# Optimization experiments

Measured on AMD Instinct MI355X. Metric: run time of the kernel, lower is better.

## Reference

```python
import jax, jax.numpy as jnp
import numpy as np

KAPPA = 5  # kNN neighbors per node (module hardcodes kappas = [5]*B, topk of KAPPA+2)


def build_graph(inputs):
    """Vectorized equivalent of get_graph(): returns flat (src, dst, edge_weight)
    over the B*S node space. Filtered kNN edges (dst < 2) are masked via weight 0,
    which is mathematically identical to removing them (gcn_norm uses edge weights)."""
    B, S, _ = inputs.shape
    diff = inputs[:, :, None, :] - inputs[:, None, :, :]            # [B,S,S,2]
    deltas = jnp.sqrt(jnp.sum(diff * diff, axis=-1))                # torch.cdist
    eye = jnp.eye(S, dtype=bool)
    d = jnp.where(eye[None], jnp.inf, deltas)                       # fill_diagonal_(inf)
    nodes = jnp.arange(2, S, dtype=jnp.int32)                       # non-depot nodes
    # depot edges: 0 -> i  and  i -> 1  for i in [2, S)
    src_dep = jnp.concatenate([jnp.zeros(S - 2, jnp.int32), nodes])
    dst_dep = jnp.concatenate([nodes, jnp.ones(S - 2, jnp.int32)])
    # kNN edges: 7 nearest per non-depot node (diag=inf so i never selected)
    _, idx = jax.lax.top_k(-d[:, 2:, :], KAPPA + 2)                 # [B, S-2, 7]
    src_knn = jnp.broadcast_to(nodes[:, None], (S - 2, KAPPA + 2)).reshape(-1)
    dst_knn = idx.reshape(B, -1).astype(jnp.int32)                  # [B, 7*(S-2)]
    mask_knn = (dst_knn >= 2).astype(jnp.float32)                   # drop depot dsts
    src = jnp.concatenate([jnp.broadcast_to(src_dep[None], (B, src_dep.shape[0])), jnp.broadcast_to(src_knn[None], (B, src_knn.shape[0]))], axis=1)
    dst = jnp.concatenate([jnp.broadcast_to(dst_dep[None], (B, dst_dep.shape[0])), dst_knn], axis=1)
    ew = jnp.concatenate([jnp.ones((B, dst_dep.shape[0]), jnp.float32), mask_knn], axis=1)
    offs = (jnp.arange(B, dtype=jnp.int32) * S)[:, None]            # batch node offset
    return (src + offs).reshape(-1), (dst + offs).reshape(-1), ew.reshape(-1)


def gcn_conv(x, src, dst, norm, self_norm, W, b, N):
    h = x @ W                                                       # GCNConv linear
    agg = jax.ops.segment_sum(h[src] * norm[:, None], dst, num_segments=N)
    agg = agg + h * self_norm[:, None]                              # self-loop term
    return agg + b


def gnn_forward(x, src, dst, ew, W0, b0, W1, b1, W2, b2):
    N = x.shape[0]
    deg = jax.ops.segment_sum(ew, dst, num_segments=N) + 1.0        # +1 self-loop
    dinv = 1.0 / jnp.sqrt(deg)
    norm = dinv[src] * dinv[dst] * ew                               # sym gcn_norm
    self_norm = dinv * dinv
    h = jax.nn.relu(gcn_conv(x, src, dst, norm, self_norm, W0, b0, N))
    h = jax.nn.relu(gcn_conv(h, src, dst, norm, self_norm, W1, b1, N))
    return gcn_conv(h, src, dst, norm, self_norm, W2, b2, N)


def setup_inputs() -> dict:
    B, S, D, H = 64, 1000, 128, 512
    key = jax.random.key(0)
    ks = jax.random.split(key, 12)
    sc = lambda fan_in: 1.0 / np.sqrt(fan_in)
    return {
        "inputs": jax.random.uniform(ks[0], (B, S, 2), jnp.float32),
        "scor": jax.random.uniform(ks[1], (B, S, 1), jnp.float32),
        "Wc": jax.random.normal(ks[2], (2, D), jnp.float32) * sc(2),
        "bc": jax.random.normal(ks[3], (D,), jnp.float32) * 0.01,
        "Ws": jax.random.normal(ks[4], (1, D), jnp.float32) * sc(1),
        "bs": jax.random.normal(ks[5], (D,), jnp.float32) * 0.01,
        "W0": jax.random.normal(ks[6], (D, H), jnp.float32) * sc(D),
        "b0": jnp.zeros((H,), jnp.float32),
        "W1": jax.random.normal(ks[8], (H, H), jnp.float32) * sc(H),
        "b1": jnp.zeros((H,), jnp.float32),
        "W2": jax.random.normal(ks[10], (H, D), jnp.float32) * sc(H),
        "b2": jnp.zeros((D,), jnp.float32),
    }


def reference(inputs, scor, Wc, bc, Ws, bs, W0, b0, W1, b1, W2, b2):
    B, S, _ = inputs.shape
    src, dst, ew = build_graph(inputs)
    x = (inputs @ Wc + bc) + (scor @ Ws + bs)                       # embedded_data
    x = x.reshape(B * S, -1)
    out = gnn_forward(x, src, dst, ew, W0, b0, W1, b1, W2, b2)
    return out.reshape(B, S, -1)
```

## Files before the change

### kernel.cpp

```cpp
#include <hip/hip_runtime.h>

typedef unsigned short u16;
typedef unsigned int u32;
typedef unsigned long long u64;
using short8 = __attribute__((ext_vector_type(8))) short;
using f32x4  = __attribute__((ext_vector_type(4))) float;

constexpr int Bb = 64, Ss = 1000, Dd = 128, Hh = 512;
constexpr int NN = Bb * Ss;
constexpr int NSRC = Ss - 2;

__device__ __forceinline__ float bf2f(u16 h) {
    u32 u = ((u32)h) << 16;
    return __builtin_bit_cast(float, u);
}
__device__ __forceinline__ u16 f2bf(float v) {
    u32 u = __builtin_bit_cast(u32, v);
    u32 r = (u + 0x7FFFu + ((u >> 16) & 1u)) >> 16;
    return (u16)r;
}
__device__ __forceinline__ float4 bf4(ushort4 v) {
    float4 r;
    r.x = bf2f(v.x); r.y = bf2f(v.y); r.z = bf2f(v.z); r.w = bf2f(v.w);
    return r;
}
__device__ __forceinline__ void gl_lds16(const void* g, void* l) {
    __builtin_amdgcn_global_load_lds(
        (const __attribute__((address_space(1))) void*)g,
        (__attribute__((address_space(3))) void*)l, 16, 0, 0);
}
__device__ __forceinline__ void acc8(float (&a)[8], uint4 v, float w) {
    u32 c[4] = {v.x, v.y, v.z, v.w};
#pragma unroll
    for (int k = 0; k < 4; ++k) {
        float lo = __builtin_bit_cast(float, c[k] << 16);
        float hi = __builtin_bit_cast(float, c[k] & 0xFFFF0000u);
        a[2 * k]     += lo * w;
        a[2 * k + 1] += hi * w;
    }
}
__device__ __forceinline__ void unp8(float (&a)[8], uint4 v) {
    u32 c[4] = {v.x, v.y, v.z, v.w};
#pragma unroll
    for (int k = 0; k < 4; ++k) {
        a[2 * k]     = __builtin_bit_cast(float, c[k] << 16);
        a[2 * k + 1] = __builtin_bit_cast(float, c[k] & 0xFFFF0000u);
    }
}

__device__ __forceinline__ u64 umin64(u64 a, u64 b) { return a < b ? a : b; }
__device__ __forceinline__ u64 umax64(u64 a, u64 b) { return a < b ? b : a; }

__device__ __forceinline__ void ins8u(u64 (&bd)[8], u64 v) {
#pragma unroll
    for (int k = 7; k >= 1; --k)
        bd[k] = umin64(umax64(v, bd[k - 1]), bd[k]);
    bd[0] = umin64(v, bd[0]);
}

__device__ __forceinline__ void merge8(u64 (&a)[8], int mask) {
    u64 b[8];
#pragma unroll
    for (int k = 0; k < 8; ++k)
        b[k] = __shfl_xor((unsigned long long)a[k], mask);
    u64 m[8];
#pragma unroll
    for (int k = 0; k < 8; ++k) m[k] = umin64(a[k], b[7 - k]);
#pragma unroll
    for (int k = 0; k < 4; ++k) {
        u64 lo = umin64(m[k], m[k + 4]), hi = umax64(m[k], m[k + 4]);
        m[k] = lo; m[k + 4] = hi;
    }
#pragma unroll
    for (int base = 0; base < 8; base += 4)
#pragma unroll
        for (int k = 0; k < 2; ++k) {
            u64 lo = umin64(m[base + k], m[base + k + 2]);
            u64 hi = umax64(m[base + k], m[base + k + 2]);
            m[base + k] = lo; m[base + k + 2] = hi;
        }
#pragma unroll
    for (int base = 0; base < 8; base += 2) {
        u64 lo = umin64(m[base], m[base + 1]), hi = umax64(m[base], m[base + 1]);
        m[base] = lo; m[base + 1] = hi;
    }
#pragma unroll
    for (int k = 0; k < 8; ++k) a[k] = m[k];
}

__global__ __launch_bounds__(256) void knn_bin_kernel(const float* __restrict__ inputs,
                                                      float2* __restrict__ gsxy,
                                                      u16* __restrict__ gsid,
                                                      int* __restrict__ gcst) {
    __shared__ float px[Ss], py[Ss];
    __shared__ int hist[256];
    __shared__ int cur[256];
    int b = blockIdx.x;
    int tid = threadIdx.x;
    const float* base = inputs + (size_t)b * Ss * 2;
    for (int t = tid; t < Ss; t += 256) { px[t] = base[2 * t]; py[t] = base[2 * t + 1]; }
    hist[tid] = 0;
    __syncthreads();
    for (int t = tid; t < Ss; t += 256) {
        int cx = min(15, (int)(px[t] * 16.0f));
        int cy = min(15, (int)(py[t] * 16.0f));
        atomicAdd(&hist[cy * 16 + cx], 1);
    }
    __syncthreads();
    int cnt = hist[tid];
    for (int s = 1; s < 256; s <<= 1) {
        int u = (tid >= s) ? hist[tid - s] : 0;
        __syncthreads();
        hist[tid] += u;
        __syncthreads();
    }
    int st = hist[tid] - cnt;
    cur[tid] = st;
    gcst[b * 260 + tid] = st;
    if (tid == 0) gcst[b * 260 + 256] = Ss;
    __syncthreads();
    for (int t = tid; t < Ss; t += 256) {
        float x = px[t], y = py[t];
        int cx = min(15, (int)(x * 16.0f));
        int cy = min(15, (int)(y * 16.0f));
        int p = atomicAdd(&cur[cy * 16 + cx], 1);
        gsxy[b * 1000 + p] = make_float2(x, y);
        gsid[b * 1000 + p] = (u16)t;
    }
}

__global__ __launch_bounds__(256) void knn_query_kernel(const float* __restrict__ inputs,
                                                        const float2* __restrict__ gsxy,
                                                        const u16* __restrict__ gsid,
                                                        const int* __restrict__ gcst,
                                                        u16* __restrict__ knn,
                                                        int* __restrict__ indeg) {
    __shared__ float2 sxy[Ss];
    __shared__ u16 sid[Ss];
    __shared__ int cst[257];
    int b = blockIdx.x;
    int tid = threadIdx.x;
    for (int t = tid; t < Ss; t += 256) { sxy[t] = gsxy[b * 1000 + t]; sid[t] = gsid[b * 1000 + t]; }
    for (int t = tid; t < 257; t += 256) cst[t] = gcst[b * 260 + t];
    __syncthreads();

    int sub = tid & 7;
    int g = tid >> 3;
    int i = 2 + blockIdx.y * 32 + g;
    if (i >= Ss) return;

    float x = inputs[(size_t)b * 2000 + 2 * i];
    float y = inputs[(size_t)b * 2000 + 2 * i + 1];
    int cx = min(15, (int)(x * 16.0f));
    int cy = min(15, (int)(y * 16.0f));
    const float INF = __builtin_inff();
    constexpr float h = 0.0625f;

    u64 bd[8];
    int w = 1;
    for (;;) {
#pragma unroll
        for (int k = 0; k < 8; ++k) bd[k] = ~0ULL;
        int x0 = max(0, cx - w), x1 = min(15, cx + w);
        int y0 = max(0, cy - w), y1 = min(15, cy + w);
        for (int cyy = y0; cyy <= y1; ++cyy) {
            int p0 = cst[cyy * 16 + x0];
            int p1 = cst[cyy * 16 + x1 + 1];
            for (int p = p0 + sub; p < p1; p += 8) {
                float2 q = sxy[p];
                int j = sid[p];
                float dx = __fsub_rn(x, q.x);
                float dy = __fsub_rn(y, q.y);
                float d2 = __fadd_rn(__fmul_rn(dx, dx), __fmul_rn(dy, dy));
                float d = __fsqrt_rn(d2);
                u64 key = (((u64)__builtin_bit_cast(u32, d)) << 32) | (u32)j;
                key = (j == i) ? ~0ULL : key;
                ins8u(bd, key);
            }
        }
        merge8(bd, 1); merge8(bd, 2); merge8(bd, 4);
        float d7 = __builtin_bit_cast(float, (u32)(bd[6] >> 32));
        float bL = (x0 > 0)  ? (x - (float)x0 * h) : INF;
        float bR = (x1 < 15) ? ((float)(x1 + 1) * h - x) : INF;
        float bB = (y0 > 0)  ? (y - (float)y0 * h) : INF;
        float bT = (y1 < 15) ? ((float)(y1 + 1) * h - y) : INF;
        float bound = fminf(fminf(bL, bR), fminf(bB, bT));
        if (d7 <= bound - 2e-6f || w >= 16) break;
        ++w;
    }

    if (sub == 0) {
        u16* kp = knn + ((size_t)b * NSRC + (i - 2)) * 7;
#pragma unroll
        for (int k = 0; k < 7; ++k) {
            int j = (int)(u32)bd[k];
            kp[k] = (u16)j;
            if (j >= 2) atomicAdd(&indeg[b * Ss + j], 1);
        }
    }
}

__global__ void deg_dinv_kernel(const int* __restrict__ indeg, float* __restrict__ dinv) {
    int n = blockIdx.x * 256 + threadIdx.x;
    if (n >= NN) return;
    int i = n % Ss;
    float deg = (i == 0) ? 1.0f : (i == 1) ? (float)(Ss - 1) : (float)(indeg[n] + 2);
    dinv[n] = 1.0f / __fsqrt_rn(deg);
}

__global__ __launch_bounds__(1024) void scan1_kernel(const int* __restrict__ indeg,
                                                     int* __restrict__ offs,
                                                     int* __restrict__ bsum) {
    __shared__ int sh[1024];
    int t = threadIdx.x;
    int idx = blockIdx.x * 1024 + t;
    int v = (idx < NN) ? indeg[idx] : 0;
    sh[t] = v;
    __syncthreads();
    for (int off = 1; off < 1024; off <<= 1) {
        int u = (t >= off) ? sh[t - off] : 0;
        __syncthreads();
        sh[t] += u;
        __syncthreads();
    }
    if (idx < NN) offs[idx] = sh[t] - v;
    if (t == 1023) bsum[blockIdx.x] = sh[1023];
}

__global__ void scan2_kernel(int* __restrict__ bsum) {
    if (threadIdx.x == 0) {
        int run = 0;
        for (int k = 0; k < 63; ++k) { int v = bsum[k]; bsum[k] = run; run += v; }
        bsum[63] = run;
    }
}

__global__ __launch_bounds__(1024) void scan3_kernel(int* __restrict__ offs,
                                                     const int* __restrict__ bsum) {
    int idx = blockIdx.x * 1024 + threadIdx.x;
    if (idx < NN) offs[idx] += bsum[blockIdx.x];
    if (idx == 0) offs[NN] = bsum[63];
}

__global__ __launch_bounds__(256) void fill_rev_kernel(const u16* __restrict__ knn,
                                                       const int* __restrict__ offs,
                                                       int* __restrict__ cursor,
                                                       u16* __restrict__ rev) {
    if (threadIdx.x >= 250) return;
    int b = blockIdx.x;
    int i = 2 + blockIdx.y * 250 + threadIdx.x;
    if (i >= Ss) return;
    const u16* kp = knn + ((size_t)b * NSRC + (i - 2)) * 7;
#pragma unroll
    for (int k = 0; k < 7; ++k) {
        int d = kp[k];
        if (d >= 2) {
            int n = b * Ss + d;
            int p = atomicAdd(&cursor[n], 1);
            rev[offs[n] + p] = (u16)i;
        }
    }
}

__global__ __launch_bounds__(512) void fuse0_kernel(const float* __restrict__ Wc,
                                                    const float* __restrict__ bc,
                                                    const float* __restrict__ Ws,
                                                    const float* __restrict__ bs,
                                                    const float* __restrict__ W0,
                                                    float* __restrict__ A) {
    int h = threadIdx.x;
    float a0 = 0.f, a1 = 0.f, a2 = 0.f, a3 = 0.f;
    for (int c = 0; c < Dd; ++c) {
        float w = W0[c * Hh + h];
        a0 += Wc[c] * w;
        a1 += Wc[Dd + c] * w;
        a2 += Ws[c] * w;
        a3 += (bc[c] + bs[c]) * w;
    }
    A[h] = a0; A[Hh + h] = a1; A[2 * Hh + h] = a2; A[3 * Hh + h] = a3;
}

__global__ __launch_bounds__(256) void gemm0f_kernel(const float* __restrict__ inputs,
                                                     const float* __restrict__ scor,
                                                     const float* __restrict__ A,
                                                     u16* __restrict__ Y) {
    int gid = blockIdx.x * 256 + threadIdx.x;
    if (gid >= NN * 128) return;
    int n = gid >> 7, t = gid & 127;
    int h = t * 4;
    float i0 = inputs[2 * n], i1 = inputs[2 * n + 1], sc = scor[n];
    float4 a0 = *(const float4*)(A + h);
    float4 a1 = *(const float4*)(A + Hh + h);
    float4 a2 = *(const float4*)(A + 2 * Hh + h);
    float4 a3 = *(const float4*)(A + 3 * Hh + h);
    ushort4 o;
    o.x = f2bf(i0 * a0.x + i1 * a1.x + sc * a2.x + a3.x);
    o.y = f2bf(i0 * a0.y + i1 * a1.y + sc * a2.y + a3.y);
    o.z = f2bf(i0 * a0.z + i1 * a1.z + sc * a2.z + a3.z);
    o.w = f2bf(i0 * a0.w + i1 * a1.w + sc * a2.w + a3.w);
    *(ushort4*)(Y + (size_t)n * Hh + h) = o;
}

__global__ void transp_kernel(const float* __restrict__ src,
                              u16* __restrict__ dst, int R, int C) {
    int gid = blockIdx.x * 256 + threadIdx.x;
    if (gid >= R * C) return;
    int r = gid / C, c = gid - r * C;
    dst[c * R + r] = f2bf(src[gid]);
}

__global__ __launch_bounds__(256) void gemm_kernel(const u16* __restrict__ A,
                                                   const u16* __restrict__ W,
                                                   u16* __restrict__ Y,
                                                   int K, int Ncols,
                                                   int nyb, int nxb) {
    __shared__ __align__(16) u16 lA[128][64];
    __shared__ __align__(16) u16 lW[128][64];

    int grp = blockIdx.x / (8 * nxb);
    int rem = blockIdx.x - grp * (8 * nxb);
    int xcd = rem & 7;
    int xb  = rem >> 3;
    int yb  = grp * 8 + xcd;
    if (yb >= nyb) return;

    int row0 = yb * 128;
    int col0 = xb * 128;
    int tid = threadIdx.x;
    int lane = tid & 63, wid = tid >> 6;
    int wm = (wid >> 1) * 64, wn = (wid & 1) * 64;
    int lanelo = lane & 15, quad = lane >> 4;

    int lrow = lane >> 3;
    int lslot = lane & 7;

    f32x4 acc[4][4] = {};

    for (int k0 = 0; k0 < K; k0 += 64) {
#pragma unroll
        for (int t = 0; t < 4; ++t) {
            int chunk = t * 4 + wid;
            int row = chunk * 8 + lrow;
            int sc = lslot ^ (row & 7);
            gl_lds16(A + (size_t)(row0 + row) * K + k0 + sc * 8, &lA[chunk * 8][0]);
        }
#pragma unroll
        for (int t = 0; t < 4; ++t) {
            int chunk = t * 4 + wid;
            int row = chunk * 8 + lrow;
            int sc = lslot ^ (row & 7);
            gl_lds16(W + (size_t)(col0 + row) * K + k0 + sc * 8, &lW[chunk * 8][0]);
        }
        __syncthreads();

#pragma unroll
        for (int kk = 0; kk < 64; kk += 32) {
            short8 af[4], bw[4];
            int cbb = (kk >> 3) + quad;
#pragma unroll
            for (int mt = 0; mt < 4; ++mt) {
                int r = wm + mt * 16 + lanelo;
                af[mt] = *(const short8*)&lA[r][((cbb ^ (r & 7))) * 8];
            }
#pragma unroll
            for (int nt = 0; nt < 4; ++nt) {
                int r = wn + nt * 16 + lanelo;
                bw[nt] = *(const short8*)&lW[r][((cbb ^ (r & 7))) * 8];
            }
#pragma unroll
            for (int mt = 0; mt < 4; ++mt)
#pragma unroll
                for (int nt = 0; nt < 4; ++nt)
                    acc[mt][nt] = __builtin_amdgcn_mfma_f32_16x16x32_bf16(
                        af[mt], bw[nt], acc[mt][nt], 0, 0, 0);
        }
        __syncthreads();
    }

#pragma unroll
    for (int mt = 0; mt < 4; ++mt)
#pragma unroll
        for (int nt = 0; nt < 4; ++nt)
#pragma unroll
            for (int r = 0; r < 4; ++r) {
                int row = row0 + wm + mt * 16 + quad * 4 + r;
                int col = col0 + wn + nt * 16 + lanelo;
                Y[(size_t)row * Ncols + col] = f2bf(acc[mt][nt][r]);
            }
}

__global__ __launch_bounds__(1024) void dep1_kernel(const u16* __restrict__ y,
                                                    const float* __restrict__ dinv,
                                                    float* __restrict__ dq,
                                                    int M) {
    int b = blockIdx.x;
    int qq = blockIdx.y;
    int co = blockIdx.z * 128;
    int tid = threadIdx.x;
    int c4 = tid & 31;
    int es = tid >> 5;
    int j0 = 2 + qq * 250;
    int j1 = j0 + 250; if (j1 > Ss) j1 = Ss;
    const u16* yb = y + (size_t)b * Ss * M + co + c4 * 4;
    const float* dv = dinv + b * Ss;
    float a0 = 0.f, a1 = 0.f, a2 = 0.f, a3 = 0.f;
    for (int j = j0 + es; j < j1; j += 32) {
        float w = dv[j];
        float4 u = bf4(*(const ushort4*)(yb + (size_t)j * M));
        a0 += u.x * w; a1 += u.y * w; a2 += u.z * w; a3 += u.w * w;
    }
    __shared__ float4 red[1024];
    float4 mv; mv.x = a0; mv.y = a1; mv.z = a2; mv.w = a3;
    red[tid] = mv;
    __syncthreads();
#pragma unroll
    for (int s = 16; s > 0; s >>= 1) {
        if (es < s) {
            float4 o = red[tid + (s << 5)];
            float4 m = red[tid];
            m.x += o.x; m.y += o.y; m.z += o.z; m.w += o.w;
            red[tid] = m;
        }
        __syncthreads();
    }
    if (es == 0)
        *(float4*)(dq + ((size_t)qq * Bb + b) * M + co + c4 * 4) = red[c4];
}

__global__ __launch_bounds__(256) void aggw512_kernel(const u16* __restrict__ y,
                                                      const float* __restrict__ dinv,
                                                      const int* __restrict__ offs,
                                                      const int* __restrict__ indeg,
                                                      const u16* __restrict__ rev,
                                                      const float* __restrict__ bias,
                                                      const float* __restrict__ dep1,
                                                      u16* __restrict__ oX) {
    int tid = threadIdx.x;
    int wv = tid >> 6, lane = tid & 63;
    int bx = blockIdx.x;
    int b = (bx & 7) + 8 * (bx / 2000);
    int i = ((bx >> 3) % 250) * 4 + wv;
    int nb = b * Ss;
    int n = nb + i;
    const u16* yB = y + (size_t)nb * 512 + lane * 8;

    float acc[8] = {};
    if (i >= 2) {
        int cnt = indeg[n], o = offs[n];
        int rv = 0; float rw = 0.f;
        if (lane < 16 && lane < cnt) { rv = rev[o + lane]; rw = dinv[nb + rv]; }
        float w0 = dinv[nb];
        uint4 v0 = *(const uint4*)yB;
        acc8(acc, v0, w0);
        int cl = cnt < 16 ? cnt : 16;
        int e = 0;
        for (; e + 4 <= cl; e += 4) {
            int   s0 = __shfl(rv, e),     s1 = __shfl(rv, e + 1);
            int   s2 = __shfl(rv, e + 2), s3 = __shfl(rv, e + 3);
            float w_0 = __shfl(rw, e),     w_1 = __shfl(rw, e + 1);
            float w_2 = __shfl(rw, e + 2), w_3 = __shfl(rw, e + 3);
            uint4 u0 = *(const uint4*)(yB + (size_t)s0 * 512);
            uint4 u1 = *(const uint4*)(yB + (size_t)s1 * 512);
            uint4 u2 = *(const uint4*)(yB + (size_t)s2 * 512);
            uint4 u3 = *(const uint4*)(yB + (size_t)s3 * 512);
            acc8(acc, u0, w_0); acc8(acc, u1, w_1);
            acc8(acc, u2, w_2); acc8(acc, u3, w_3);
        }
        for (; e < cl; ++e) {
            int s = __shfl(rv, e); float ww = __shfl(rw, e);
            uint4 u = *(const uint4*)(yB + (size_t)s * 512);
            acc8(acc, u, ww);
        }
        for (; e < cnt; ++e) {
            int s = rev[o + e]; float ww = dinv[nb + s];
            uint4 u = *(const uint4*)(yB + (size_t)s * 512);
            acc8(acc, u, ww);
        }
    } else if (i == 1) {
        const float* dp = dep1 + (size_t)b * 512 + lane * 8;
#pragma unroll
        for (int qq = 0; qq < 4; ++qq) {
            float4 v0 = *(const float4*)(dp + (size_t)qq * Bb * 512);
            float4 v1 = *(const float4*)(dp + (size_t)qq * Bb * 512 + 4);
            acc[0] += v0.x; acc[1] += v0.y; acc[2] += v0.z; acc[3] += v0.w;
            acc[4] += v1.x; acc[5] += v1.y; acc[6] += v1.z; acc[7] += v1.w;
        }
    }
    float dn = dinv[n], sn = dn * dn;
    float s8[8];
    unp8(s8, *(const uint4*)(yB + (size_t)i * 512));
    float4 bl = *(const float4*)(bias + lane * 8);
    float4 bh = *(const float4*)(bias + lane * 8 + 4);
    float bz[8] = {bl.x, bl.y, bl.z, bl.w, bh.x, bh.y, bh.z, bh.w};
    u32 ow[4];
#pragma unroll
    for (int k = 0; k < 4; ++k) {
        float z0 = acc[2 * k]     * dn + s8[2 * k]     * sn + bz[2 * k];
        float z1 = acc[2 * k + 1] * dn + s8[2 * k + 1] * sn + bz[2 * k + 1];
        ow[k] = (u32)f2bf(fmaxf(z0, 0.f)) | ((u32)f2bf(fmaxf(z1, 0.f)) << 16);
    }
    uint4 ov = {ow[0], ow[1], ow[2], ow[3]};
    *(uint4*)(oX + (size_t)n * 512 + lane * 8) = ov;
}

__global__ __launch_bounds__(128) void agg128f_kernel(const u16* __restrict__ y,
                                                      const float* __restrict__ dinv,
                                                      const int* __restrict__ offs,
                                                      const int* __restrict__ indeg,
                                                      const u16* __restrict__ rev,
                                                      const float* __restrict__ bias,
                                                      const float* __restrict__ dep1,
                                                      float* __restrict__ out) {
    int bx = blockIdx.x;
    int x = bx & 7, q = bx >> 3;
    int bb = q / 1000;
    int i = q - bb * 1000;
    int b = x + (bb << 3);
    int n = b * Ss + i;
    int nb = n - i;
    int tid = threadIdx.x, c = tid;

    __shared__ int   sidx[128];
    __shared__ float sw[128];
    int cnt = 0, o = 0;
    if (i >= 2) { cnt = indeg[n]; o = offs[n]; }
    int cl = cnt < 128 ? cnt : 128;
    if (tid < cl) {
        int s = rev[o + tid];
        sidx[tid] = s;
        sw[tid] = dinv[nb + s];
    }
    __syncthreads();

    float a = 0.f;
    if (i >= 2) {
        a = bf2f(y[(size_t)nb * 128 + c]) * dinv[nb];
        int e = 0;
        for (; e + 4 <= cl; e += 4) {
            int s0 = sidx[e], s1 = sidx[e + 1], s2 = sidx[e + 2], s3 = sidx[e + 3];
            float w0 = sw[e], w1 = sw[e + 1], w2 = sw[e + 2], w3 = sw[e + 3];
            float u0 = bf2f(y[(size_t)(nb + s0) * 128 + c]);
            float u1 = bf2f(y[(size_t)(nb + s1) * 128 + c]);
            float u2 = bf2f(y[(size_t)(nb + s2) * 128 + c]);
            float u3 = bf2f(y[(size_t)(nb + s3) * 128 + c]);
            a += u0 * w0 + u1 * w1 + u2 * w2 + u3 * w3;
        }
        for (; e < cl; ++e) a += bf2f(y[(size_t)(nb + sidx[e]) * 128 + c]) * sw[e];
        for (int e2 = 128; e2 < cnt; ++e2) {
            int s = rev[o + e2];
            a += bf2f(y[(size_t)(nb + s) * 128 + c]) * dinv[nb + s];
        }
    } else if (i == 1) {
#pragma unroll
        for (int qq = 0; qq < 4; ++qq)
            a += dep1[((size_t)qq * Bb + b) * 128 + c];
    }
    float dn = dinv[n];
    out[(size_t)n * 128 + c] = a * dn + bf2f(y[(size_t)n * 128 + c]) * (dn * dn) + bias[c];
}

constexpr size_t O_INDEG  = 0;
constexpr size_t O_CURSOR = 256000;
constexpr size_t O_OFFS   = 512000;
constexpr size_t O_DINV   = 768256;
constexpr size_t O_KNN    = 1024256;
constexpr size_t O_REV    = 1918080;
constexpr size_t O_AMAT   = 2811904;
constexpr size_t O_WT1    = 2942976;
constexpr size_t O_WT2    = 3467264;
constexpr size_t O_X      = 3598336;
constexpr size_t O_Y      = 69134336;
constexpr size_t O_DEP1A  = 134670336;
constexpr size_t O_DEP1B  = 135194624;
constexpr size_t O_BSUM   = 135325696;
constexpr size_t O_GSXY   = O_X;
constexpr size_t O_GSID   = O_X + 512000;
constexpr size_t O_GCST   = O_X + 640000;

extern "C" void kernel_launch(void* const* d_in, const int* in_sizes, int n_in,
                              void* d_out, int out_size, void* d_ws, size_t ws_size,
                              hipStream_t stream) {
    const float* inputs = (const float*)d_in[0];
    const float* scor   = (const float*)d_in[1];
    const float* Wc     = (const float*)d_in[2];
    const float* bc     = (const float*)d_in[3];
    const float* Ws     = (const float*)d_in[4];
    const float* bs     = (const float*)d_in[5];
    const float* W0     = (const float*)d_in[6];
    const float* b0     = (const float*)d_in[7];
    const float* W1     = (const float*)d_in[8];
    const float* b1     = (const float*)d_in[9];
    const float* W2     = (const float*)d_in[10];
    const float* b2     = (const float*)d_in[11];

    char* w = (char*)d_ws;
    int*    indeg  = (int*)(w + O_INDEG);
    int*    cursor = (int*)(w + O_CURSOR);
    int*    offs   = (int*)(w + O_OFFS);
    float*  dinv   = (float*)(w + O_DINV);
    u16*    knn    = (u16*)(w + O_KNN);
    u16*    rev    = (u16*)(w + O_REV);
    float*  amat   = (float*)(w + O_AMAT);
    u16*    wt1    = (u16*)(w + O_WT1);
    u16*    wt2    = (u16*)(w + O_WT2);
    u16*    xbf    = (u16*)(w + O_X);
    u16*    ybf    = (u16*)(w + O_Y);
    float*  dep1a  = (float*)(w + O_DEP1A);
    float*  dep1b  = (float*)(w + O_DEP1B);
    int*    bsum   = (int*)(w + O_BSUM);
    float2* gsxy   = (float2*)(w + O_GSXY);
    u16*    gsid   = (u16*)(w + O_GSID);
    int*    gcst   = (int*)(w + O_GCST);

    hipMemsetAsync(w + O_INDEG, 0, 512000, stream);

    knn_bin_kernel<<<Bb, 256, 0, stream>>>(inputs, gsxy, gsid, gcst);
    knn_query_kernel<<<dim3(Bb, 32), 256, 0, stream>>>(inputs, gsxy, gsid, gcst, knn, indeg);
    deg_dinv_kernel<<<250, 256, 0, stream>>>(indeg, dinv);
    scan1_kernel<<<63, 1024, 0, stream>>>(indeg, offs, bsum);
    scan2_kernel<<<1, 64, 0, stream>>>(bsum);
    scan3_kernel<<<63, 1024, 0, stream>>>(offs, bsum);
    fill_rev_kernel<<<dim3(Bb, 4), 256, 0, stream>>>(knn, offs, cursor, rev);

    fuse0_kernel<<<1, 512, 0, stream>>>(Wc, bc, Ws, bs, W0, amat);
    transp_kernel<<<(Hh * Hh + 255) / 256, 256, 0, stream>>>(W1, wt1, Hh, Hh);
    transp_kernel<<<(Hh * Dd + 255) / 256, 256, 0, stream>>>(W2, wt2, Hh, Dd);

    gemm0f_kernel<<<NN * 128 / 256, 256, 0, stream>>>(inputs, scor, amat, ybf);
    dep1_kernel<<<dim3(Bb, 4, 4), 1024, 0, stream>>>(ybf, dinv, dep1a, Hh);
    aggw512_kernel<<<NN / 4, 256, 0, stream>>>(ybf, dinv, offs, indeg, rev, b0, dep1a, xbf);
    gemm_kernel<<<63 * 32, 256, 0, stream>>>(xbf, wt1, ybf, Hh, Hh, 500, 4);
    dep1_kernel<<<dim3(Bb, 4, 4), 1024, 0, stream>>>(ybf, dinv, dep1a, Hh);
    aggw512_kernel<<<NN / 4, 256, 0, stream>>>(ybf, dinv, offs, indeg, rev, b1, dep1a, xbf);
    gemm_kernel<<<63 * 8, 256, 0, stream>>>(xbf, wt2, ybf, Hh, Dd, 500, 1);
    dep1_kernel<<<dim3(Bb, 4, 1), 1024, 0, stream>>>(ybf, dinv, dep1b, Dd);
    agg128f_kernel<<<NN, 128, 0, stream>>>(ybf, dinv, offs, indeg, rev, b2, dep1b, (float*)d_out);
}
```

Measured before the change: 381.5 us.

## Aggregate 4-dim embedding before expanding to 512 for first GCN layer

Layer-0 features are an affine map of three scalars per node, and aggregation is linear. The new code aggregates the 4-component vector (inputs, score, 1) over graph edges first, then expands it through the fused 4x512 matrix with bias and ReLU. This replaces the 512-wide gather, the dep1 pass and the bf16 write/read of the pre-aggregation features with a small per-batch kernel and one expansion kernel. The per-batch aggregation runs only 64 blocks, and the intermediate is now kept in fp32 rather than bf16, which slightly changes the numerics.

New measurement: 338.5 us. 11.3% less time.

```diff
diff --git a/kernel.cpp b/kernel.cpp
--- a/kernel.cpp
+++ b/kernel.cpp
@@ -280,25 +280,98 @@
     A[h] = a0; A[Hh + h] = a1; A[2 * Hh + h] = a2; A[3 * Hh + h] = a3;
 }
 
-__global__ __launch_bounds__(256) void gemm0f_kernel(const float* __restrict__ inputs,
+__global__ __launch_bounds__(1024) void agg_e_kernel(const float* __restrict__ inputs,
                                                      const float* __restrict__ scor,
-                                                     const float* __restrict__ A,
-                                                     u16* __restrict__ Y) {
+                                                     const float* __restrict__ dinv,
+                                                     const int* __restrict__ offs,
+                                                     const int* __restrict__ indeg,
+                                                     const u16* __restrict__ rev,
+                                                     float4* __restrict__ ve) {
+    __shared__ float se0[Ss], se1[Ss], se2[Ss], sdv[Ss];
+    __shared__ float4 depw[16];
+    int b = blockIdx.x;
+    int tid = threadIdx.x;
+    int nb = b * Ss;
+    const float* base = inputs + (size_t)nb * 2;
+    for (int t = tid; t < Ss; t += 1024) {
+        se0[t] = base[2 * t];
+        se1[t] = base[2 * t + 1];
+        se2[t] = scor[nb + t];
+        sdv[t] = dinv[nb + t];
+    }
+    __syncthreads();
+
+    float4 dep = {0.f, 0.f, 0.f, 0.f};
+    for (int r = tid; r < Ss; r += 1024) {
+        if (r >= 2) {
+            float w = sdv[r];
+            dep.x += se0[r] * w; dep.y += se1[r] * w;
+            dep.z += se2[r] * w; dep.w += w;
+        }
+    }
+#pragma unroll
+    for (int m = 1; m < 64; m <<= 1) {
+        dep.x += __shfl_xor(dep.x, m);
+        dep.y += __shfl_xor(dep.y, m);
+        dep.z += __shfl_xor(dep.z, m);
+        dep.w += __shfl_xor(dep.w, m);
+    }
+    if ((tid & 63) == 0) depw[tid >> 6] = dep;
+    __syncthreads();
+
+    int i = tid;
+    if (i >= Ss) return;
+    float dn = sdv[i], sn = dn * dn;
+    float4 acc = {0.f, 0.f, 0.f, 0.f};
+    if (i >= 2) {
+        int n = nb + i;
+        int cnt = indeg[n], o = offs[n];
+        float w0 = sdv[0];
+        acc.x = se0[0] * w0; acc.y = se1[0] * w0;
+        acc.z = se2[0] * w0; acc.w = w0;
+        for (int e = 0; e < cnt; ++e) {
+            int s = rev[o + e];
+            float w = sdv[s];
+            acc.x += se0[s] * w; acc.y += se1[s] * w;
+            acc.z += se2[s] * w; acc.w += w;
+        }
+    } else if (i == 1) {
+        float4 t = {0.f, 0.f, 0.f, 0.f};
+#pragma unroll
+        for (int k = 0; k < 16; ++k) {
+            t.x += depw[k].x; t.y += depw[k].y;
+            t.z += depw[k].z; t.w += depw[k].w;
+        }
+        acc = t;
+    }
+    float4 v;
+    v.x = acc.x * dn + se0[i] * sn;
+    v.y = acc.y * dn + se1[i] * sn;
+    v.z = acc.z * dn + se2[i] * sn;
+    v.w = acc.w * dn + sn;
+    ve[nb + i] = v;
+}
+
+__global__ __launch_bounds__(256) void expand512_kernel(const float4* __restrict__ ve,
+                                                        const float* __restrict__ A,
+                                                        const float* __restrict__ bias,
+                                                        u16* __restrict__ X) {
     int gid = blockIdx.x * 256 + threadIdx.x;
     if (gid >= NN * 128) return;
     int n = gid >> 7, t = gid & 127;
     int h = t * 4;
-    float i0 = inputs[2 * n], i1 = inputs[2 * n + 1], sc = scor[n];
+    float4 v = ve[n];
     float4 a0 = *(const float4*)(A + h);
     float4 a1 = *(const float4*)(A + Hh + h);
     float4 a2 = *(const float4*)(A + 2 * Hh + h);
     float4 a3 = *(const float4*)(A + 3 * Hh + h);
+    float4 bz = *(const float4*)(bias + h);
     ushort4 o;
-    o.x = f2bf(i0 * a0.x + i1 * a1.x + sc * a2.x + a3.x);
-    o.y = f2bf(i0 * a0.y + i1 * a1.y + sc * a2.y + a3.y);
-    o.z = f2bf(i0 * a0.z + i1 * a1.z + sc * a2.z + a3.z);
-    o.w = f2bf(i0 * a0.w + i1 * a1.w + sc * a2.w + a3.w);
-    *(ushort4*)(Y + (size_t)n * Hh + h) = o;
+    o.x = f2bf(fmaxf(v.x * a0.x + v.y * a1.x + v.z * a2.x + v.w * a3.x + bz.x, 0.f));
+    o.y = f2bf(fmaxf(v.x * a0.y + v.y * a1.y + v.z * a2.y + v.w * a3.y + bz.y, 0.f));
+    o.z = f2bf(fmaxf(v.x * a0.z + v.y * a1.z + v.z * a2.z + v.w * a3.z + bz.z, 0.f));
+    o.w = f2bf(fmaxf(v.x * a0.w + v.y * a1.w + v.z * a2.w + v.w * a3.w + bz.w, 0.f));
+    *(ushort4*)(X + (size_t)n * Hh + h) = o;
 }
 
 __global__ void transp_kernel(const float* __restrict__ src,
@@ -576,6 +649,7 @@
 constexpr size_t O_GSXY   = O_X;
 constexpr size_t O_GSID   = O_X + 512000;
 constexpr size_t O_GCST   = O_X + 640000;
+constexpr size_t O_VE     = O_Y;
 
 extern "C" void kernel_launch(void* const* d_in, const int* in_sizes, int n_in,
                               void* d_out, int out_size, void* d_ws, size_t ws_size,
@@ -611,6 +685,7 @@
     float2* gsxy   = (float2*)(w + O_GSXY);
     u16*    gsid   = (u16*)(w + O_GSID);
     int*    gcst   = (int*)(w + O_GCST);
+    float4* ve     = (float4*)(w + O_VE);
 
     hipMemsetAsync(w + O_INDEG, 0, 512000, stream);
 
@@ -626,9 +701,8 @@
     transp_kernel<<<(Hh * Hh + 255) / 256, 256, 0, stream>>>(W1, wt1, Hh, Hh);
     transp_kernel<<<(Hh * Dd + 255) / 256, 256, 0, stream>>>(W2, wt2, Hh, Dd);
 
-    gemm0f_kernel<<<NN * 128 / 256, 256, 0, stream>>>(inputs, scor, amat, ybf);
-    dep1_kernel<<<dim3(Bb, 4, 4), 1024, 0, stream>>>(ybf, dinv, dep1a, Hh);
-    aggw512_kernel<<<NN / 4, 256, 0, stream>>>(ybf, dinv, offs, indeg, rev, b0, dep1a, xbf);
+    agg_e_kernel<<<Bb, 1024, 0, stream>>>(inputs, scor, dinv, offs, indeg, rev, ve);
+    expand512_kernel<<<NN * 128 / 256, 256, 0, stream>>>(ve, amat, b0, xbf);
     gemm_kernel<<<63 * 32, 256, 0, stream>>>(xbf, wt1, ybf, Hh, Hh, 500, 4);
     dep1_kernel<<<dim3(Bb, 4, 4), 1024, 0, stream>>>(ybf, dinv, dep1a, Hh);
     aggw512_kernel<<<NN / 4, 256, 0, stream>>>(ybf, dinv, offs, indeg, rev, b1, dep1a, xbf);
```
